# Optimization experiments

Hardware: AMD Instinct MI355X
Metric: run time of the kernel (lower is better)

## Reference

```python
import jax, jax.numpy as jnp
import numpy as np

N = 50000      # nodes
E = 1_600_000  # edges
IN, H, H2, OUT = 256, 128, 64, 2
EPS = 1e-5     # BatchNorm eps


def setup_inputs() -> dict:
    key = jax.random.key(0)
    ks = jax.random.split(key, 18)
    inp = {
        "x": jax.random.normal(ks[0], (N, IN), dtype=jnp.float32),
        "edge_index": jax.random.randint(ks[1], (2, E), 0, N, dtype=jnp.int64),
        # GCNConv 1
        "W1": jax.random.normal(ks[2], (IN, H), dtype=jnp.float32) / np.sqrt(IN),
        "b1": jnp.zeros((H,), dtype=jnp.float32),
        "g1": jnp.ones((H,), dtype=jnp.float32),
        "be1": jnp.zeros((H,), dtype=jnp.float32),
        "m1": jax.random.normal(ks[3], (H,), dtype=jnp.float32) * 0.1,
        "v1": jax.random.uniform(ks[4], (H,), dtype=jnp.float32, minval=0.5, maxval=1.5),
        # GCNConv 2
        "W2": jax.random.normal(ks[5], (H, H2), dtype=jnp.float32) / np.sqrt(H),
        "b2": jnp.zeros((H2,), dtype=jnp.float32),
        "g2": jnp.ones((H2,), dtype=jnp.float32),
        "be2": jnp.zeros((H2,), dtype=jnp.float32),
        "m2": jax.random.normal(ks[6], (H2,), dtype=jnp.float32) * 0.1,
        "v2": jax.random.uniform(ks[7], (H2,), dtype=jnp.float32, minval=0.5, maxval=1.5),
        # final linear
        "Wl": jax.random.normal(ks[8], (H2, OUT), dtype=jnp.float32) / np.sqrt(H2),
        "bl": jnp.zeros((OUT,), dtype=jnp.float32),
    }
    return inp


def _gcn_conv(x, W, b, src, dst, n_nodes):
    # PyG GCNConv: linear transform, then symmetric-normalized aggregation
    # with self-loops (gcn_norm, improved=False, fill_value=1).
    xw = x @ W                                            # [N, H]
    ones = jnp.ones((src.shape[0],), dtype=x.dtype)
    deg = jax.ops.segment_sum(ones, dst, num_segments=n_nodes) + 1.0  # +1 self-loop
    dinv = jax.lax.rsqrt(deg)                             # deg^{-1/2}
    norm = dinv[src] * dinv[dst]                          # [E]
    msgs = xw[src] * norm[:, None]                        # [E, H] gather
    agg = jax.ops.segment_sum(msgs, dst, num_segments=n_nodes)  # scatter-add
    agg = agg + xw * (1.0 / deg)[:, None]                 # self-loop term
    return agg + b


def _bn_relu(x, gamma, beta, mean, var):
    # inference-mode BatchNorm1d + ReLU
    xhat = (x - mean) * jax.lax.rsqrt(var + EPS)
    return jax.nn.relu(xhat * gamma + beta)


def reference(x, edge_index, W1, b1, g1, be1, m1, v1,
              W2, b2, g2, be2, m2, v2, Wl, bl):
    src, dst = edge_index[0], edge_index[1]
    h = _gcn_conv(x, W1, b1, src, dst, N)
    h = _bn_relu(h, g1, be1, m1, v1)
    # dropout is identity in eval mode
    h = _gcn_conv(h, W2, b2, src, dst, N)
    h = _bn_relu(h, g2, be2, m2, v2)
    return h @ Wl + bl
```

## Files before the change

kernel.cpp:

```cpp
#include <hip/hip_runtime.h>

#define N_NODES 50000
#define N_EDGES 1600000
#define IN_F 256
#define H1_F 128
#define H2_F 64
#define OUT_F 2
#define BN_EPS 1e-5f

#define NBUK 782
#define BCAP 3584
#define CHUNK 4096
#define NCHUNK 391
#define NPW 8

typedef __attribute__((ext_vector_type(8))) short bf16x8;
typedef __attribute__((ext_vector_type(4))) float f32x4;
typedef __attribute__((ext_vector_type(4))) int   i32x4;
typedef __attribute__((ext_vector_type(4))) unsigned u32x4;

__device__ __forceinline__ unsigned short f2b(float f) {
    union { float f; unsigned u; } v; v.f = f;
    unsigned r = (v.u + 0x7FFFu + ((v.u >> 16) & 1u)) >> 16;
    return (unsigned short)r;
}
__device__ __forceinline__ float b2f(unsigned short b) {
    union { unsigned u; float f; } v; v.u = ((unsigned)b) << 16;
    return v.f;
}
__device__ __forceinline__ void add2(float& a0, float& a1, unsigned u) {
    union { unsigned u; float f; } lo, hi;
    lo.u = u << 16;
    hi.u = u & 0xFFFF0000u;
    a0 += lo.f; a1 += hi.f;
}

__launch_bounds__(256)
__global__ void chist_kernel(const int* __restrict__ dst, int* __restrict__ h,
                             int* __restrict__ tot) {
    __shared__ int lh[NBUK];
    const int c = blockIdx.x;
    for (int i = threadIdx.x; i < NBUK; i += 256) lh[i] = 0;
    __syncthreads();
    const int e0 = c * CHUNK;
    const int e1 = min(e0 + CHUNK, N_EDGES);
    const i32x4* p = (const i32x4*)(dst + e0);
    const int n4 = (e1 - e0) >> 2;
    for (int i = threadIdx.x; i < n4; i += 256) {
        i32x4 d = __builtin_nontemporal_load(p + i);
        atomicAdd(&lh[d.x >> 6], 1);
        atomicAdd(&lh[d.y >> 6], 1);
        atomicAdd(&lh[d.z >> 6], 1);
        atomicAdd(&lh[d.w >> 6], 1);
    }
    __syncthreads();
    for (int i = threadIdx.x; i < NBUK; i += 256) {
        int v = lh[i];
        h[(size_t)i * NCHUNK + c] = v;
        if (v) atomicAdd(&tot[i], v);
    }
}

__global__ void bscan_kernel(const int* __restrict__ tot, int* __restrict__ boff,
                             int* __restrict__ rowptr) {
    __shared__ int tmp[1024];
    const int t = threadIdx.x;
    int v = (t < NBUK) ? tot[t] : 0;
    tmp[t] = v;
    __syncthreads();
    for (int off = 1; off < 1024; off <<= 1) {
        int a = (t >= off) ? tmp[t - off] : 0;
        __syncthreads();
        tmp[t] += a;
        __syncthreads();
    }
    if (t < NBUK) boff[t] = tmp[t] - v;
    if (t == 0) { boff[NBUK] = N_EDGES; rowptr[N_NODES] = N_EDGES; }
}

__launch_bounds__(256)
__global__ void boffs_kernel(int* __restrict__ h, const int* __restrict__ boff) {
    const int b = (blockIdx.x * blockDim.x + threadIdx.x) >> 6;
    if (b >= NBUK) return;
    const int lane = threadIdx.x & 63;
    int run = boff[b];
    int* row = h + (size_t)b * NCHUNK;
    for (int c0 = 0; c0 < NCHUNK; c0 += 64) {
        int idx = c0 + lane;
        int v = (idx < NCHUNK) ? row[idx] : 0;
        int s = v;
#pragma unroll
        for (int off = 1; off < 64; off <<= 1) {
            int t = __shfl_up(s, off);
            if (lane >= off) s += t;
        }
        if (idx < NCHUNK) row[idx] = run + (s - v);
        run += __shfl(s, 63);
    }
}

__launch_bounds__(256)
__global__ void cscatter_kernel(const int* __restrict__ src, const int* __restrict__ dst,
                                const int* __restrict__ h, unsigned* __restrict__ bedges) {
    __shared__ int cur[NBUK];
    const int c = blockIdx.x;
    for (int i = threadIdx.x; i < NBUK; i += 256) cur[i] = h[(size_t)i * NCHUNK + c];
    __syncthreads();
    const int e0 = c * CHUNK;
    const int e1 = min(e0 + CHUNK, N_EDGES);
    const i32x4* pd = (const i32x4*)(dst + e0);
    const i32x4* ps = (const i32x4*)(src + e0);
    const int n4 = (e1 - e0) >> 2;
    for (int i = threadIdx.x; i < n4; i += 256) {
        i32x4 d = __builtin_nontemporal_load(pd + i);
        i32x4 s = __builtin_nontemporal_load(ps + i);
        int slot;
        slot = atomicAdd(&cur[d.x >> 6], 1); bedges[slot] = (unsigned)s.x | ((unsigned)d.x << 16);
        slot = atomicAdd(&cur[d.y >> 6], 1); bedges[slot] = (unsigned)s.y | ((unsigned)d.y << 16);
        slot = atomicAdd(&cur[d.z >> 6], 1); bedges[slot] = (unsigned)s.z | ((unsigned)d.z << 16);
        slot = atomicAdd(&cur[d.w >> 6], 1); bedges[slot] = (unsigned)s.w | ((unsigned)d.w << 16);
    }
}

__launch_bounds__(256)
__global__ void build_kernel(const unsigned* __restrict__ bedges, const int* __restrict__ boff,
                             unsigned short* __restrict__ perm, int* __restrict__ rowptr,
                             float* __restrict__ dinv) {
    __shared__ unsigned e_lds[BCAP];
    __shared__ unsigned short p_lds[BCAP];
    __shared__ int ncnt[64], ncur[64];

    const int b = blockIdx.x;
    const int t = threadIdx.x;
    const int start = boff[b];
    const int end   = boff[b + 1];
    const int cnt   = end - start;
    const bool fits = (cnt <= BCAP);

    if (t < 64) ncnt[t] = 0;
    __syncthreads();

    for (int i = t; i < cnt; i += 256) {
        unsigned e = bedges[start + i];
        if (fits) e_lds[i] = e;
        atomicAdd(&ncnt[(e >> 16) & 63], 1);
    }
    __syncthreads();

    if (t == 0) {
        int a = 0;
        for (int i = 0; i < 64; ++i) { ncur[i] = a; a += ncnt[i]; }
    }
    __syncthreads();

    if (t < 64) {
        int node = b * 64 + t;
        if (node < N_NODES) {
            rowptr[node] = start + ncur[t];
            dinv[node]   = rsqrtf((float)ncnt[t] + 1.0f);
        }
    }
    __syncthreads();

    for (int i = t; i < cnt; i += 256) {
        unsigned e = fits ? e_lds[i] : bedges[start + i];
        int slot = atomicAdd(&ncur[(e >> 16) & 63], 1);
        unsigned short s = (unsigned short)(e & 0xFFFFu);
        if (fits) p_lds[slot] = s;
        else      perm[start + slot] = s;
    }
    if (fits) {
        __syncthreads();
        for (int i = t; i < cnt; i += 256) perm[start + i] = p_lds[i];
    }
}

__global__ void prep_kernel(const float* __restrict__ W1, const float* __restrict__ W2,
                            unsigned short* __restrict__ w1t, unsigned short* __restrict__ w2t,
                            const float* __restrict__ g1, const float* __restrict__ be1,
                            const float* __restrict__ m1, const float* __restrict__ v1,
                            const float* __restrict__ b1,
                            const float* __restrict__ g2, const float* __restrict__ be2,
                            const float* __restrict__ m2, const float* __restrict__ v2,
                            const float* __restrict__ b2,
                            float* __restrict__ sc1, float* __restrict__ sh1,
                            float* __restrict__ sc2, float* __restrict__ sh2) {
    const int blk = blockIdx.x;
    const int t = threadIdx.x;
    if (blk < 128) {
        int i = blk * 256 + t;
        int n = i / IN_F, k = i % IN_F;
        w1t[i] = f2b(W1[(size_t)k * H1_F + n]);
    } else if (blk < 160) {
        int i = (blk - 128) * 256 + t;
        int n = i / H1_F, k = i % H1_F;
        w2t[i] = f2b(W2[(size_t)k * H2_F + n]);
    } else {
        if (t < H1_F) {
            float s = g1[t] * rsqrtf(v1[t] + BN_EPS);
            sc1[t] = s;
            sh1[t] = (b1[t] - m1[t]) * s + be1[t];
        } else if (t < H1_F + H2_F) {
            int f = t - H1_F;
            float s = g2[f] * rsqrtf(v2[f] + BN_EPS);
            sc2[f] = s;
            sh2[f] = (b2[f] - m2[f]) * s + be2[f];
        }
    }
}

template <int KSTEPS, int NTILES, bool A_BF16>
__launch_bounds__(256)
__global__ void mfma_gemm_kernel(const void* __restrict__ Ap, const unsigned short* __restrict__ BT,
                                 const float* __restrict__ dscale, unsigned short* __restrict__ C,
                                 int M) {
    constexpr int K  = KSTEPS * 32;
    constexpr int NF = NTILES * 16;
    const int wave = threadIdx.x >> 6;
    const int lane = threadIdx.x & 63;
    const int r0   = (blockIdx.x * 4 + wave) * 16;
    const int m    = lane & 15;
    const int kb   = lane >> 4;

    int arow = r0 + m;
    if (arow >= M) arow = M - 1;

    f32x4 acc[NTILES];
#pragma unroll
    for (int nt = 0; nt < NTILES; ++nt) acc[nt] = (f32x4)(0.f);

#pragma unroll
    for (int ks = 0; ks < KSTEPS; ++ks) {
        const int k0 = ks * 32 + kb * 8;
        bf16x8 a;
        if constexpr (A_BF16) {
            a = *(const bf16x8*)((const unsigned short*)Ap + (size_t)arow * K + k0);
        } else {
            const float* af = (const float*)Ap + (size_t)arow * K + k0;
            f32x4 lo = __builtin_nontemporal_load((const f32x4*)af);
            f32x4 hi = __builtin_nontemporal_load((const f32x4*)(af + 4));
            union { bf16x8 v; unsigned short u[8]; } pk;
            pk.u[0] = f2b(lo.x); pk.u[1] = f2b(lo.y); pk.u[2] = f2b(lo.z); pk.u[3] = f2b(lo.w);
            pk.u[4] = f2b(hi.x); pk.u[5] = f2b(hi.y); pk.u[6] = f2b(hi.z); pk.u[7] = f2b(hi.w);
            a = pk.v;
        }
#pragma unroll
        for (int nt = 0; nt < NTILES; ++nt) {
            bf16x8 b = *(const bf16x8*)(BT + (size_t)(nt * 16 + m) * K + k0);
            acc[nt] = __builtin_amdgcn_mfma_f32_16x16x32_bf16(a, b, acc[nt], 0, 0, 0);
        }
    }

#pragma unroll
    for (int reg = 0; reg < 4; ++reg) {
        const int r = r0 + kb * 4 + reg;
        if (r < M) {
            const float ds = dscale[r];
#pragma unroll
            for (int nt = 0; nt < NTILES; ++nt)
                C[(size_t)r * NF + nt * 16 + m] = f2b(acc[nt][reg] * ds);
        }
    }
}

template <int HF, bool FINAL>
__launch_bounds__(256)
__global__ void agg_kernel(const int* __restrict__ rowptr, const unsigned short* __restrict__ perm,
                           const unsigned short* __restrict__ xw, const float* __restrict__ dinv,
                           const float* __restrict__ sc, const float* __restrict__ sh,
                           const float* __restrict__ Wl, const float* __restrict__ bl,
                           void* __restrict__ outp) {
    constexpr int LPE = HF / 8;
    constexpr int G   = 64 / LPE;
    const int wid  = (blockIdx.x * blockDim.x + threadIdx.x) >> 6;
    const int n0   = wid * NPW;
    if (n0 >= N_NODES) return;
    const int lane = threadIdx.x & 63;
    const int grp  = lane / LPE;
    const int fl   = (lane % LPE) * 8;

    f32x4 scl = *(const f32x4*)(sc + fl);
    f32x4 sch = *(const f32x4*)(sc + fl + 4);
    f32x4 shl = *(const f32x4*)(sh + fl);
    f32x4 shh = *(const f32x4*)(sh + fl + 4);
    float wl0[8], wl1[8];
    if constexpr (FINAL) {
#pragma unroll
        for (int i = 0; i < 8; ++i) {
            wl0[i] = Wl[(fl + i) * 2 + 0];
            wl1[i] = Wl[(fl + i) * 2 + 1];
        }
    }

    int rp = 0;
    if (lane <= NPW) rp = rowptr[n0 + lane];
    float dvl = (lane < NPW) ? dinv[n0 + lane] : 0.f;

    for (int k = 0; k < NPW; ++k) {
        const int node  = n0 + k;
        const int start = __shfl(rp, k);
        const int end   = __shfl(rp, k + 1);

        float aA[8];
#pragma unroll
        for (int i = 0; i < 8; ++i) aA[i] = 0.f;

        if (grp == 0) {
            u32x4 u = *(const u32x4*)(xw + (size_t)node * HF + fl);
#pragma unroll
            for (int i = 0; i < 4; ++i) add2(aA[2 * i], aA[2 * i + 1], u[i]);
        }

        for (int base = start; base < end; base += 64) {
            int pidx = base + lane;
            int pv = (int)__builtin_nontemporal_load(perm + (pidx < end ? pidx : end - 1));
            int ne = end - base;
            if (ne > 64) ne = 64;
            if (ne == 64) {
#pragma unroll
                for (int j = 0; j < 64; j += G) {
                    int s = __shfl(pv, j + grp);
                    u32x4 u = *(const u32x4*)(xw + (size_t)s * HF + fl);
#pragma unroll
                    for (int i = 0; i < 4; ++i) add2(aA[2 * i], aA[2 * i + 1], u[i]);
                }
            } else {
                for (int j = 0; j < ne; j += G) {
                    int s = __shfl(pv, j + grp);
                    if (j + grp < ne) {
                        u32x4 u = *(const u32x4*)(xw + (size_t)s * HF + fl);
#pragma unroll
                        for (int i = 0; i < 4; ++i) add2(aA[2 * i], aA[2 * i + 1], u[i]);
                    }
                }
            }
        }

#pragma unroll
        for (int off = LPE; off < 64; off <<= 1)
#pragma unroll
            for (int i = 0; i < 8; ++i) aA[i] += __shfl_xor(aA[i], off);

        const float dv = __shfl(dvl, k);
        float y[8];
#pragma unroll
        for (int i = 0; i < 4; ++i) {
            y[i]     = fmaxf(aA[i] * (dv * scl[i]) + shl[i], 0.f);
            y[i + 4] = fmaxf(aA[i + 4] * (dv * sch[i]) + shh[i], 0.f);
        }

        if constexpr (!FINAL) {
            if (lane < LPE) {
                u32x4 o;
#pragma unroll
                for (int i = 0; i < 4; ++i)
                    o[i] = (unsigned)f2b(y[2 * i]) | ((unsigned)f2b(y[2 * i + 1]) << 16);
                __builtin_nontemporal_store(o, (u32x4*)((unsigned short*)outp + (size_t)node * HF + fl));
            }
        } else {
            float p0 = 0.f, p1 = 0.f;
#pragma unroll
            for (int i = 0; i < 8; ++i) {
                p0 += y[i] * wl0[i];
                p1 += y[i] * wl1[i];
            }
#pragma unroll
            for (int off = 1; off < LPE; off <<= 1) {
                p0 += __shfl_xor(p0, off);
                p1 += __shfl_xor(p1, off);
            }
            if (lane == 0) {
                float* o = (float*)outp;
                o[(size_t)node * 2 + 0] = p0 + bl[0];
                o[(size_t)node * 2 + 1] = p1 + bl[1];
            }
        }
    }
}

extern "C" void kernel_launch(void* const* d_in, const int* in_sizes, int n_in,
                              void* d_out, int out_size, void* d_ws, size_t ws_size,
                              hipStream_t stream) {
    const float* x   = (const float*)d_in[0];
    const int*   ei  = (const int*)d_in[1];
    const float* W1  = (const float*)d_in[2];
    const float* b1  = (const float*)d_in[3];
    const float* g1  = (const float*)d_in[4];
    const float* be1 = (const float*)d_in[5];
    const float* m1  = (const float*)d_in[6];
    const float* v1  = (const float*)d_in[7];
    const float* W2  = (const float*)d_in[8];
    const float* b2  = (const float*)d_in[9];
    const float* g2  = (const float*)d_in[10];
    const float* be2 = (const float*)d_in[11];
    const float* m2  = (const float*)d_in[12];
    const float* v2  = (const float*)d_in[13];
    const float* Wl  = (const float*)d_in[14];
    const float* bl  = (const float*)d_in[15];

    const int* src = ei;
    const int* dst = ei + N_EDGES;

    int*            h      = (int*)d_ws;
    int*            tot    = h + (size_t)NBUK * NCHUNK;
    int*            boff   = tot + 1024;
    int*            rowptr = boff + 1024;
    float*          dinv   = (float*)(rowptr + 50016);
    float*          sc1    = dinv + 50016;
    float*          sh1    = sc1 + 128;
    float*          sc2    = sh1 + 128;
    float*          sh2    = sc2 + 64;
    unsigned*       bedges = (unsigned*)(sh2 + 64);
    unsigned short* perm   = (unsigned short*)(bedges + N_EDGES);
    unsigned short* xwb    = perm + N_EDGES;
    unsigned short* h1b    = xwb + (size_t)N_NODES * H1_F;
    unsigned short* w1t    = h1b + (size_t)N_NODES * H1_F;
    unsigned short* w2t    = w1t + H1_F * IN_F;

    hipMemsetAsync(tot, 0, 1024 * sizeof(int), stream);

    chist_kernel<<<NCHUNK, 256, 0, stream>>>(dst, h, tot);
    bscan_kernel<<<1, 1024, 0, stream>>>(tot, boff, rowptr);
    boffs_kernel<<<(NBUK * 64 + 255) / 256, 256, 0, stream>>>(h, boff);
    cscatter_kernel<<<NCHUNK, 256, 0, stream>>>(src, dst, h, bedges);
    build_kernel<<<NBUK, 256, 0, stream>>>(bedges, boff, perm, rowptr, dinv);

    prep_kernel<<<161, 256, 0, stream>>>(W1, W2, w1t, w2t,
                                         g1, be1, m1, v1, b1,
                                         g2, be2, m2, v2, b2,
                                         sc1, sh1, sc2, sh2);

    mfma_gemm_kernel<IN_F / 32, H1_F / 16, false><<<(N_NODES + 63) / 64, 256, 0, stream>>>(
        x, w1t, dinv, xwb, N_NODES);
    agg_kernel<H1_F, false><<<(N_NODES / NPW + 3) / 4, 256, 0, stream>>>(
        rowptr, perm, xwb, dinv, sc1, sh1, nullptr, nullptr, h1b);

    mfma_gemm_kernel<H1_F / 32, H2_F / 16, true><<<(N_NODES + 63) / 64, 256, 0, stream>>>(
        h1b, w2t, dinv, xwb, N_NODES);
    agg_kernel<H2_F, true><<<(N_NODES / NPW + 3) / 4, 256, 0, stream>>>(
        rowptr, perm, xwb, dinv, sc2, sh2, Wl, bl, (float*)d_out);
}
```

Before: 299.7 us.

## Split layer-1 features into 32-wide chunks for cache-resident gather aggregation

The first GEMM now writes its output in a feature-chunked layout (four 32-feature planes of N×32 bf16), and the layer-1 aggregation runs one grid slice per chunk, so each pass gathers from a ~3.2MB table that fits in cache better. The second GEMM reads this chunked layout directly. Both aggregation kernels switch from 8 nodes per wave to one node per wave. The cost is that edge indices (perm/rowptr) are read four times for layer 1, and with only ~32 edges per node many lanes sit idle per wave.

```diff
diff --git a/kernel.cpp b/kernel.cpp
--- a/kernel.cpp
+++ b/kernel.cpp
@@ -12,7 +12,7 @@
 #define BCAP 3584
 #define CHUNK 4096
 #define NCHUNK 391
-#define NPW 8
+#define FC 32
 
 typedef __attribute__((ext_vector_type(8))) short bf16x8;
 typedef __attribute__((ext_vector_type(4))) float f32x4;
@@ -209,7 +209,7 @@
     }
 }
 
-template <int KSTEPS, int NTILES, bool A_BF16>
+template <int KSTEPS, int NTILES, bool A_CHUNKED, bool CHUNK_OUT>
 __launch_bounds__(256)
 __global__ void mfma_gemm_kernel(const void* __restrict__ Ap, const unsigned short* __restrict__ BT,
                                  const float* __restrict__ dscale, unsigned short* __restrict__ C,
@@ -233,8 +233,9 @@
     for (int ks = 0; ks < KSTEPS; ++ks) {
         const int k0 = ks * 32 + kb * 8;
         bf16x8 a;
-        if constexpr (A_BF16) {
-            a = *(const bf16x8*)((const unsigned short*)Ap + (size_t)arow * K + k0);
+        if constexpr (A_CHUNKED) {
+            a = *(const bf16x8*)((const unsigned short*)Ap +
+                                 (size_t)ks * N_NODES * FC + (size_t)arow * FC + kb * 8);
         } else {
             const float* af = (const float*)Ap + (size_t)arow * K + k0;
             f32x4 lo = __builtin_nontemporal_load((const f32x4*)af);
@@ -257,124 +258,180 @@
         if (r < M) {
             const float ds = dscale[r];
 #pragma unroll
-            for (int nt = 0; nt < NTILES; ++nt)
-                C[(size_t)r * NF + nt * 16 + m] = f2b(acc[nt][reg] * ds);
-        }
-    }
-}
-
-template <int HF, bool FINAL>
-__launch_bounds__(256)
-__global__ void agg_kernel(const int* __restrict__ rowptr, const unsigned short* __restrict__ perm,
-                           const unsigned short* __restrict__ xw, const float* __restrict__ dinv,
-                           const float* __restrict__ sc, const float* __restrict__ sh,
-                           const float* __restrict__ Wl, const float* __restrict__ bl,
-                           void* __restrict__ outp) {
-    constexpr int LPE = HF / 8;
-    constexpr int G   = 64 / LPE;
-    const int wid  = (blockIdx.x * blockDim.x + threadIdx.x) >> 6;
-    const int n0   = wid * NPW;
-    if (n0 >= N_NODES) return;
+            for (int nt = 0; nt < NTILES; ++nt) {
+                if constexpr (CHUNK_OUT) {
+                    C[(size_t)(nt >> 1) * N_NODES * FC + (size_t)r * FC + ((nt & 1) << 4) + m] =
+                        f2b(acc[nt][reg] * ds);
+                } else {
+                    C[(size_t)r * NF + nt * 16 + m] = f2b(acc[nt][reg] * ds);
+                }
+            }
+        }
+    }
+}
+
+__launch_bounds__(256)
+__global__ void agg_chunk_kernel(const int* __restrict__ rowptr, const unsigned short* __restrict__ perm,
+                                 const unsigned short* __restrict__ xw,
+                                 const float* __restrict__ dinv,
+                                 const float* __restrict__ sc, const float* __restrict__ sh,
+                                 unsigned short* __restrict__ out) {
+    const int c = blockIdx.y;
+    const unsigned short* xc = xw + (size_t)c * N_NODES * FC;
+    const int wave = threadIdx.x >> 6;
+    const int node = blockIdx.x * 4 + wave;
+    if (node >= N_NODES) return;
+    const int lane = threadIdx.x & 63;
+    const int grp  = lane >> 2;
+    const int fl   = (lane & 3) << 3;
+
+    float aA[8];
+#pragma unroll
+    for (int i = 0; i < 8; ++i) aA[i] = 0.f;
+
+    if (grp == 0) {
+        u32x4 u = *(const u32x4*)(xc + (size_t)node * FC + fl);
+#pragma unroll
+        for (int i = 0; i < 4; ++i) add2(aA[2 * i], aA[2 * i + 1], u[i]);
+    }
+
+    const int start = rowptr[node];
+    const int end   = rowptr[node + 1];
+    for (int base = start; base < end; base += 64) {
+        int pidx = base + lane;
+        int pv = (int)__builtin_nontemporal_load(perm + (pidx < end ? pidx : end - 1));
+        int ne = end - base;
+        if (ne > 64) ne = 64;
+        if (ne == 64) {
+#pragma unroll
+            for (int j = 0; j < 64; j += 16) {
+                int s = __shfl(pv, j + grp);
+                u32x4 u = *(const u32x4*)(xc + (size_t)s * FC + fl);
+#pragma unroll
+                for (int i = 0; i < 4; ++i) add2(aA[2 * i], aA[2 * i + 1], u[i]);
+            }
+        } else {
+            for (int j = 0; j < ne; j += 16) {
+                int s = __shfl(pv, j + grp);
+                if (j + grp < ne) {
+                    u32x4 u = *(const u32x4*)(xc + (size_t)s * FC + fl);
+#pragma unroll
+                    for (int i = 0; i < 4; ++i) add2(aA[2 * i], aA[2 * i + 1], u[i]);
+                }
+            }
+        }
+    }
+
+#pragma unroll
+    for (int off = 4; off < 64; off <<= 1)
+#pragma unroll
+        for (int i = 0; i < 8; ++i) aA[i] += __shfl_xor(aA[i], off);
+
+    if (lane < 4) {
+        const float dv = dinv[node];
+        const int f = c * FC + fl;
+        f32x4 scl = *(const f32x4*)(sc + f);
+        f32x4 sch = *(const f32x4*)(sc + f + 4);
+        f32x4 shl = *(const f32x4*)(sh + f);
+        f32x4 shh = *(const f32x4*)(sh + f + 4);
+        float y[8];
+#pragma unroll
+        for (int i = 0; i < 4; ++i) {
+            y[i]     = fmaxf(aA[i] * (dv * scl[i]) + shl[i], 0.f);
+            y[i + 4] = fmaxf(aA[i + 4] * (dv * sch[i]) + shh[i], 0.f);
+        }
+        u32x4 o;
+#pragma unroll
+        for (int i = 0; i < 4; ++i)
+            o[i] = (unsigned)f2b(y[2 * i]) | ((unsigned)f2b(y[2 * i + 1]) << 16);
+        __builtin_nontemporal_store(o, (u32x4*)(out + (size_t)c * N_NODES * FC + (size_t)node * FC + fl));
+    }
+}
+
+__launch_bounds__(256)
+__global__ void agg_final_kernel(const int* __restrict__ rowptr, const unsigned short* __restrict__ perm,
+                                 const unsigned short* __restrict__ xw, const float* __restrict__ dinv,
+                                 const float* __restrict__ sc, const float* __restrict__ sh,
+                                 const float* __restrict__ Wl, const float* __restrict__ bl,
+                                 float* __restrict__ outp) {
+    constexpr int HF  = 64;
+    constexpr int LPE = 8;
+    constexpr int G   = 8;
+    const int wave = threadIdx.x >> 6;
+    const int node = blockIdx.x * 4 + wave;
+    if (node >= N_NODES) return;
     const int lane = threadIdx.x & 63;
     const int grp  = lane / LPE;
     const int fl   = (lane % LPE) * 8;
 
+    float aA[8];
+#pragma unroll
+    for (int i = 0; i < 8; ++i) aA[i] = 0.f;
+
+    if (grp == 0) {
+        u32x4 u = *(const u32x4*)(xw + (size_t)node * HF + fl);
+#pragma unroll
+        for (int i = 0; i < 4; ++i) add2(aA[2 * i], aA[2 * i + 1], u[i]);
+    }
+
+    const int start = rowptr[node];
+    const int end   = rowptr[node + 1];
+    for (int base = start; base < end; base += 64) {
+        int pidx = base + lane;
+        int pv = (int)__builtin_nontemporal_load(perm + (pidx < end ? pidx : end - 1));
+        int ne = end - base;
+        if (ne > 64) ne = 64;
+        if (ne == 64) {
+#pragma unroll
+            for (int j = 0; j < 64; j += G) {
+                int s = __shfl(pv, j + grp);
+                u32x4 u = *(const u32x4*)(xw + (size_t)s * HF + fl);
+#pragma unroll
+                for (int i = 0; i < 4; ++i) add2(aA[2 * i], aA[2 * i + 1], u[i]);
+            }
+        } else {
+            for (int j = 0; j < ne; j += G) {
+                int s = __shfl(pv, j + grp);
+                if (j + grp < ne) {
+                    u32x4 u = *(const u32x4*)(xw + (size_t)s * HF + fl);
+#pragma unroll
+                    for (int i = 0; i < 4; ++i) add2(aA[2 * i], aA[2 * i + 1], u[i]);
+                }
+            }
+        }
+    }
+
+#pragma unroll
+    for (int off = LPE; off < 64; off <<= 1)
+#pragma unroll
+        for (int i = 0; i < 8; ++i) aA[i] += __shfl_xor(aA[i], off);
+
+    const float dv = dinv[node];
     f32x4 scl = *(const f32x4*)(sc + fl);
     f32x4 sch = *(const f32x4*)(sc + fl + 4);
     f32x4 shl = *(const f32x4*)(sh + fl);
     f32x4 shh = *(const f32x4*)(sh + fl + 4);
-    float wl0[8], wl1[8];
-    if constexpr (FINAL) {
-#pragma unroll
-        for (int i = 0; i < 8; ++i) {
-            wl0[i] = Wl[(fl + i) * 2 + 0];
-            wl1[i] = Wl[(fl + i) * 2 + 1];
-        }
-    }
-
-    int rp = 0;
-    if (lane <= NPW) rp = rowptr[n0 + lane];
-    float dvl = (lane < NPW) ? dinv[n0 + lane] : 0.f;
-
-    for (int k = 0; k < NPW; ++k) {
-        const int node  = n0 + k;
-        const int start = __shfl(rp, k);
-        const int end   = __shfl(rp, k + 1);
-
-        float aA[8];
-#pragma unroll
-        for (int i = 0; i < 8; ++i) aA[i] = 0.f;
-
-        if (grp == 0) {
-            u32x4 u = *(const u32x4*)(xw + (size_t)node * HF + fl);
-#pragma unroll
-            for (int i = 0; i < 4; ++i) add2(aA[2 * i], aA[2 * i + 1], u[i]);
-        }
-
-        for (int base = start; base < end; base += 64) {
-            int pidx = base + lane;
-            int pv = (int)__builtin_nontemporal_load(perm + (pidx < end ? pidx : end - 1));
-            int ne = end - base;
-            if (ne > 64) ne = 64;
-            if (ne == 64) {
-#pragma unroll
-                for (int j = 0; j < 64; j += G) {
-                    int s = __shfl(pv, j + grp);
-                    u32x4 u = *(const u32x4*)(xw + (size_t)s * HF + fl);
-#pragma unroll
-                    for (int i = 0; i < 4; ++i) add2(aA[2 * i], aA[2 * i + 1], u[i]);
-                }
-            } else {
-                for (int j = 0; j < ne; j += G) {
-                    int s = __shfl(pv, j + grp);
-                    if (j + grp < ne) {
-                        u32x4 u = *(const u32x4*)(xw + (size_t)s * HF + fl);
-#pragma unroll
-                        for (int i = 0; i < 4; ++i) add2(aA[2 * i], aA[2 * i + 1], u[i]);
-                    }
-                }
-            }
-        }
-
-#pragma unroll
-        for (int off = LPE; off < 64; off <<= 1)
-#pragma unroll
-            for (int i = 0; i < 8; ++i) aA[i] += __shfl_xor(aA[i], off);
-
-        const float dv = __shfl(dvl, k);
-        float y[8];
-#pragma unroll
-        for (int i = 0; i < 4; ++i) {
-            y[i]     = fmaxf(aA[i] * (dv * scl[i]) + shl[i], 0.f);
-            y[i + 4] = fmaxf(aA[i + 4] * (dv * sch[i]) + shh[i], 0.f);
-        }
-
-        if constexpr (!FINAL) {
-            if (lane < LPE) {
-                u32x4 o;
-#pragma unroll
-                for (int i = 0; i < 4; ++i)
-                    o[i] = (unsigned)f2b(y[2 * i]) | ((unsigned)f2b(y[2 * i + 1]) << 16);
-                __builtin_nontemporal_store(o, (u32x4*)((unsigned short*)outp + (size_t)node * HF + fl));
-            }
-        } else {
-            float p0 = 0.f, p1 = 0.f;
-#pragma unroll
-            for (int i = 0; i < 8; ++i) {
-                p0 += y[i] * wl0[i];
-                p1 += y[i] * wl1[i];
-            }
-#pragma unroll
-            for (int off = 1; off < LPE; off <<= 1) {
-                p0 += __shfl_xor(p0, off);
-                p1 += __shfl_xor(p1, off);
-            }
-            if (lane == 0) {
-                float* o = (float*)outp;
-                o[(size_t)node * 2 + 0] = p0 + bl[0];
-                o[(size_t)node * 2 + 1] = p1 + bl[1];
-            }
-        }
+    float y[8];
+#pragma unroll
+    for (int i = 0; i < 4; ++i) {
+        y[i]     = fmaxf(aA[i] * (dv * scl[i]) + shl[i], 0.f);
+        y[i + 4] = fmaxf(aA[i + 4] * (dv * sch[i]) + shh[i], 0.f);
+    }
+
+    float p0 = 0.f, p1 = 0.f;
+#pragma unroll
+    for (int i = 0; i < 8; ++i) {
+        p0 += y[i] * Wl[(fl + i) * 2 + 0];
+        p1 += y[i] * Wl[(fl + i) * 2 + 1];
+    }
+#pragma unroll
+    for (int off = 1; off < LPE; off <<= 1) {
+        p0 += __shfl_xor(p0, off);
+        p1 += __shfl_xor(p1, off);
+    }
+    if (lane == 0) {
+        outp[(size_t)node * 2 + 0] = p0 + bl[0];
+        outp[(size_t)node * 2 + 1] = p1 + bl[1];
     }
 }
 
@@ -430,13 +487,13 @@
                                          g2, be2, m2, v2, b2,
                                          sc1, sh1, sc2, sh2);
 
-    mfma_gemm_kernel<IN_F / 32, H1_F / 16, false><<<(N_NODES + 63) / 64, 256, 0, stream>>>(
+    mfma_gemm_kernel<IN_F / 32, H1_F / 16, false, true><<<(N_NODES + 63) / 64, 256, 0, stream>>>(
         x, w1t, dinv, xwb, N_NODES);
-    agg_kernel<H1_F, false><<<(N_NODES / NPW + 3) / 4, 256, 0, stream>>>(
-        rowptr, perm, xwb, dinv, sc1, sh1, nullptr, nullptr, h1b);
-
-    mfma_gemm_kernel<H1_F / 32, H2_F / 16, true><<<(N_NODES + 63) / 64, 256, 0, stream>>>(
+    agg_chunk_kernel<<<dim3((N_NODES + 3) / 4, H1_F / FC), 256, 0, stream>>>(
+        rowptr, perm, xwb, dinv, sc1, sh1, h1b);
+
+    mfma_gemm_kernel<H1_F / 32, H2_F / 16, true, false><<<(N_NODES + 63) / 64, 256, 0, stream>>>(
         h1b, w2t, dinv, xwb, N_NODES);
-    agg_kernel<H2_F, true><<<(N_NODES / NPW + 3) / 4, 256, 0, stream>>>(
+    agg_final_kernel<<<(N_NODES + 3) / 4, 256, 0, stream>>>(
         rowptr, perm, xwb, dinv, sc2, sh2, Wl, bl, (float*)d_out);
 }
```

Measured after the change: 287.2 us. -4.2%, faster.

## Fuse histogram with weight prep, merge bucket scan, one node per wave in aggregation

Applied to the files above, without the earlier changes.

The weight transpose/BN-constant prep blocks are merged into the histogram launch, and the single-block bucket scan is folded into the per-bucket offset kernel, where each wave recomputes its own exclusive prefix from the totals. The aggregation kernels now assign one node per wave instead of eight nodes per wave, giving more waves and better latency hiding for the irregular gathers. This removes two launches and a serial scan stage. In exchange it adds redundant prefix reads in each wave and per-wave overhead for rowptr, dinv and scale loads.

```diff
diff --git a/kernel.cpp b/kernel.cpp
--- a/kernel.cpp
+++ b/kernel.cpp
@@ -12,7 +12,6 @@
 #define BCAP 3584
 #define CHUNK 4096
 #define NCHUNK 391
-#define NPW 8
 
 typedef __attribute__((ext_vector_type(8))) short bf16x8;
 typedef __attribute__((ext_vector_type(4))) float f32x4;
@@ -36,54 +35,83 @@
 }
 
 __launch_bounds__(256)
-__global__ void chist_kernel(const int* __restrict__ dst, int* __restrict__ h,
-                             int* __restrict__ tot) {
-    __shared__ int lh[NBUK];
-    const int c = blockIdx.x;
-    for (int i = threadIdx.x; i < NBUK; i += 256) lh[i] = 0;
-    __syncthreads();
-    const int e0 = c * CHUNK;
-    const int e1 = min(e0 + CHUNK, N_EDGES);
-    const i32x4* p = (const i32x4*)(dst + e0);
-    const int n4 = (e1 - e0) >> 2;
-    for (int i = threadIdx.x; i < n4; i += 256) {
-        i32x4 d = __builtin_nontemporal_load(p + i);
-        atomicAdd(&lh[d.x >> 6], 1);
-        atomicAdd(&lh[d.y >> 6], 1);
-        atomicAdd(&lh[d.z >> 6], 1);
-        atomicAdd(&lh[d.w >> 6], 1);
-    }
-    __syncthreads();
-    for (int i = threadIdx.x; i < NBUK; i += 256) {
-        int v = lh[i];
-        h[(size_t)i * NCHUNK + c] = v;
-        if (v) atomicAdd(&tot[i], v);
-    }
-}
-
-__global__ void bscan_kernel(const int* __restrict__ tot, int* __restrict__ boff,
-                             int* __restrict__ rowptr) {
-    __shared__ int tmp[1024];
-    const int t = threadIdx.x;
-    int v = (t < NBUK) ? tot[t] : 0;
-    tmp[t] = v;
-    __syncthreads();
-    for (int off = 1; off < 1024; off <<= 1) {
-        int a = (t >= off) ? tmp[t - off] : 0;
+__global__ void chist_prep_kernel(const int* __restrict__ dst, int* __restrict__ h,
+                                  int* __restrict__ tot,
+                                  const float* __restrict__ W1, const float* __restrict__ W2,
+                                  unsigned short* __restrict__ w1t, unsigned short* __restrict__ w2t,
+                                  const float* __restrict__ g1, const float* __restrict__ be1,
+                                  const float* __restrict__ m1, const float* __restrict__ v1,
+                                  const float* __restrict__ b1,
+                                  const float* __restrict__ g2, const float* __restrict__ be2,
+                                  const float* __restrict__ m2, const float* __restrict__ v2,
+                                  const float* __restrict__ b2,
+                                  float* __restrict__ sc1, float* __restrict__ sh1,
+                                  float* __restrict__ sc2, float* __restrict__ sh2) {
+    const int blk = blockIdx.x;
+    const int t   = threadIdx.x;
+    if (blk < NCHUNK) {
+        __shared__ int lh[NBUK];
+        const int c = blk;
+        for (int i = t; i < NBUK; i += 256) lh[i] = 0;
         __syncthreads();
-        tmp[t] += a;
+        const int e0 = c * CHUNK;
+        const int e1 = min(e0 + CHUNK, N_EDGES);
+        const i32x4* p = (const i32x4*)(dst + e0);
+        const int n4 = (e1 - e0) >> 2;
+        for (int i = t; i < n4; i += 256) {
+            i32x4 d = __builtin_nontemporal_load(p + i);
+            atomicAdd(&lh[d.x >> 6], 1);
+            atomicAdd(&lh[d.y >> 6], 1);
+            atomicAdd(&lh[d.z >> 6], 1);
+            atomicAdd(&lh[d.w >> 6], 1);
+        }
         __syncthreads();
-    }
-    if (t < NBUK) boff[t] = tmp[t] - v;
-    if (t == 0) { boff[NBUK] = N_EDGES; rowptr[N_NODES] = N_EDGES; }
-}
-
-__launch_bounds__(256)
-__global__ void boffs_kernel(int* __restrict__ h, const int* __restrict__ boff) {
+        for (int i = t; i < NBUK; i += 256) {
+            int v = lh[i];
+            h[(size_t)i * NCHUNK + c] = v;
+            if (v) atomicAdd(&tot[i], v);
+        }
+    } else {
+        const int blk2 = blk - NCHUNK;
+        if (blk2 < 128) {
+            int i = blk2 * 256 + t;
+            int n = i / IN_F, k = i % IN_F;
+            w1t[i] = f2b(W1[(size_t)k * H1_F + n]);
+        } else if (blk2 < 160) {
+            int i = (blk2 - 128) * 256 + t;
+            int n = i / H1_F, k = i % H1_F;
+            w2t[i] = f2b(W2[(size_t)k * H2_F + n]);
+        } else {
+            if (t < H1_F) {
+                float s = g1[t] * rsqrtf(v1[t] + BN_EPS);
+                sc1[t] = s;
+                sh1[t] = (b1[t] - m1[t]) * s + be1[t];
+            } else if (t < H1_F + H2_F) {
+                int f = t - H1_F;
+                float s = g2[f] * rsqrtf(v2[f] + BN_EPS);
+                sc2[f] = s;
+                sh2[f] = (b2[f] - m2[f]) * s + be2[f];
+            }
+        }
+    }
+}
+
+__launch_bounds__(256)
+__global__ void scanoffs_kernel(const int* __restrict__ tot, int* __restrict__ boff,
+                                int* __restrict__ h, int* __restrict__ rowptr) {
     const int b = (blockIdx.x * blockDim.x + threadIdx.x) >> 6;
     if (b >= NBUK) return;
     const int lane = threadIdx.x & 63;
-    int run = boff[b];
+
+    int acc = 0;
+    for (int i = lane; i < NBUK; i += 64)
+        if (i < b) acc += tot[i];
+#pragma unroll
+    for (int off = 1; off < 64; off <<= 1) acc += __shfl_xor(acc, off);
+    if (lane == 0) boff[b] = acc;
+    if (b == 0 && lane == 0) { boff[NBUK] = N_EDGES; rowptr[N_NODES] = N_EDGES; }
+
+    int run = acc;
     int* row = h + (size_t)b * NCHUNK;
     for (int c0 = 0; c0 < NCHUNK; c0 += 64) {
         int idx = c0 + lane;
@@ -91,8 +119,8 @@
         int s = v;
 #pragma unroll
         for (int off = 1; off < 64; off <<= 1) {
-            int t = __shfl_up(s, off);
-            if (lane >= off) s += t;
+            int t2 = __shfl_up(s, off);
+            if (lane >= off) s += t2;
         }
         if (idx < NCHUNK) row[idx] = run + (s - v);
         run += __shfl(s, 63);
@@ -175,40 +203,6 @@
     }
 }
 
-__global__ void prep_kernel(const float* __restrict__ W1, const float* __restrict__ W2,
-                            unsigned short* __restrict__ w1t, unsigned short* __restrict__ w2t,
-                            const float* __restrict__ g1, const float* __restrict__ be1,
-                            const float* __restrict__ m1, const float* __restrict__ v1,
-                            const float* __restrict__ b1,
-                            const float* __restrict__ g2, const float* __restrict__ be2,
-                            const float* __restrict__ m2, const float* __restrict__ v2,
-                            const float* __restrict__ b2,
-                            float* __restrict__ sc1, float* __restrict__ sh1,
-                            float* __restrict__ sc2, float* __restrict__ sh2) {
-    const int blk = blockIdx.x;
-    const int t = threadIdx.x;
-    if (blk < 128) {
-        int i = blk * 256 + t;
-        int n = i / IN_F, k = i % IN_F;
-        w1t[i] = f2b(W1[(size_t)k * H1_F + n]);
-    } else if (blk < 160) {
-        int i = (blk - 128) * 256 + t;
-        int n = i / H1_F, k = i % H1_F;
-        w2t[i] = f2b(W2[(size_t)k * H2_F + n]);
-    } else {
-        if (t < H1_F) {
-            float s = g1[t] * rsqrtf(v1[t] + BN_EPS);
-            sc1[t] = s;
-            sh1[t] = (b1[t] - m1[t]) * s + be1[t];
-        } else if (t < H1_F + H2_F) {
-            int f = t - H1_F;
-            float s = g2[f] * rsqrtf(v2[f] + BN_EPS);
-            sc2[f] = s;
-            sh2[f] = (b2[f] - m2[f]) * s + be2[f];
-        }
-    }
-}
-
 template <int KSTEPS, int NTILES, bool A_BF16>
 __launch_bounds__(256)
 __global__ void mfma_gemm_kernel(const void* __restrict__ Ap, const unsigned short* __restrict__ BT,
@@ -272,108 +266,91 @@
                            void* __restrict__ outp) {
     constexpr int LPE = HF / 8;
     constexpr int G   = 64 / LPE;
-    const int wid  = (blockIdx.x * blockDim.x + threadIdx.x) >> 6;
-    const int n0   = wid * NPW;
-    if (n0 >= N_NODES) return;
+    const int wave = threadIdx.x >> 6;
+    const int node = blockIdx.x * 4 + wave;
+    if (node >= N_NODES) return;
     const int lane = threadIdx.x & 63;
     const int grp  = lane / LPE;
     const int fl   = (lane % LPE) * 8;
 
+    float aA[8];
+#pragma unroll
+    for (int i = 0; i < 8; ++i) aA[i] = 0.f;
+
+    if (grp == 0) {
+        u32x4 u = *(const u32x4*)(xw + (size_t)node * HF + fl);
+#pragma unroll
+        for (int i = 0; i < 4; ++i) add2(aA[2 * i], aA[2 * i + 1], u[i]);
+    }
+
+    const int start = rowptr[node];
+    const int end   = rowptr[node + 1];
+    for (int base = start; base < end; base += 64) {
+        int pidx = base + lane;
+        int pv = (int)__builtin_nontemporal_load(perm + (pidx < end ? pidx : end - 1));
+        int ne = end - base;
+        if (ne > 64) ne = 64;
+        if (ne == 64) {
+#pragma unroll
+            for (int j = 0; j < 64; j += G) {
+                int s = __shfl(pv, j + grp);
+                u32x4 u = *(const u32x4*)(xw + (size_t)s * HF + fl);
+#pragma unroll
+                for (int i = 0; i < 4; ++i) add2(aA[2 * i], aA[2 * i + 1], u[i]);
+            }
+        } else {
+            for (int j = 0; j < ne; j += G) {
+                int s = __shfl(pv, j + grp);
+                if (j + grp < ne) {
+                    u32x4 u = *(const u32x4*)(xw + (size_t)s * HF + fl);
+#pragma unroll
+                    for (int i = 0; i < 4; ++i) add2(aA[2 * i], aA[2 * i + 1], u[i]);
+                }
+            }
+        }
+    }
+
+#pragma unroll
+    for (int off = LPE; off < 64; off <<= 1)
+#pragma unroll
+        for (int i = 0; i < 8; ++i) aA[i] += __shfl_xor(aA[i], off);
+
+    const float dv = dinv[node];
     f32x4 scl = *(const f32x4*)(sc + fl);
     f32x4 sch = *(const f32x4*)(sc + fl + 4);
     f32x4 shl = *(const f32x4*)(sh + fl);
     f32x4 shh = *(const f32x4*)(sh + fl + 4);
-    float wl0[8], wl1[8];
-    if constexpr (FINAL) {
+    float y[8];
+#pragma unroll
+    for (int i = 0; i < 4; ++i) {
+        y[i]     = fmaxf(aA[i] * (dv * scl[i]) + shl[i], 0.f);
+        y[i + 4] = fmaxf(aA[i + 4] * (dv * sch[i]) + shh[i], 0.f);
+    }
+
+    if constexpr (!FINAL) {
+        if (lane < LPE) {
+            u32x4 o;
+#pragma unroll
+            for (int i = 0; i < 4; ++i)
+                o[i] = (unsigned)f2b(y[2 * i]) | ((unsigned)f2b(y[2 * i + 1]) << 16);
+            __builtin_nontemporal_store(o, (u32x4*)((unsigned short*)outp + (size_t)node * HF + fl));
+        }
+    } else {
+        float p0 = 0.f, p1 = 0.f;
 #pragma unroll
         for (int i = 0; i < 8; ++i) {
-            wl0[i] = Wl[(fl + i) * 2 + 0];
-            wl1[i] = Wl[(fl + i) * 2 + 1];
-        }
-    }
-
-    int rp = 0;
-    if (lane <= NPW) rp = rowptr[n0 + lane];
-    float dvl = (lane < NPW) ? dinv[n0 + lane] : 0.f;
-
-    for (int k = 0; k < NPW; ++k) {
-        const int node  = n0 + k;
-        const int start = __shfl(rp, k);
-        const int end   = __shfl(rp, k + 1);
-
-        float aA[8];
-#pragma unroll
-        for (int i = 0; i < 8; ++i) aA[i] = 0.f;
-
-        if (grp == 0) {
-            u32x4 u = *(const u32x4*)(xw + (size_t)node * HF + fl);
-#pragma unroll
-            for (int i = 0; i < 4; ++i) add2(aA[2 * i], aA[2 * i + 1], u[i]);
-        }
-
-        for (int base = start; base < end; base += 64) {
-            int pidx = base + lane;
-            int pv = (int)__builtin_nontemporal_load(perm + (pidx < end ? pidx : end - 1));
-            int ne = end - base;
-            if (ne > 64) ne = 64;
-            if (ne == 64) {
-#pragma unroll
-                for (int j = 0; j < 64; j += G) {
-                    int s = __shfl(pv, j + grp);
-                    u32x4 u = *(const u32x4*)(xw + (size_t)s * HF + fl);
-#pragma unroll
-                    for (int i = 0; i < 4; ++i) add2(aA[2 * i], aA[2 * i + 1], u[i]);
-                }
-            } else {
-                for (int j = 0; j < ne; j += G) {
-                    int s = __shfl(pv, j + grp);
-                    if (j + grp < ne) {
-                        u32x4 u = *(const u32x4*)(xw + (size_t)s * HF + fl);
-#pragma unroll
-                        for (int i = 0; i < 4; ++i) add2(aA[2 * i], aA[2 * i + 1], u[i]);
-                    }
-                }
-            }
-        }
-
-#pragma unroll
-        for (int off = LPE; off < 64; off <<= 1)
-#pragma unroll
-            for (int i = 0; i < 8; ++i) aA[i] += __shfl_xor(aA[i], off);
-
-        const float dv = __shfl(dvl, k);
-        float y[8];
-#pragma unroll
-        for (int i = 0; i < 4; ++i) {
-            y[i]     = fmaxf(aA[i] * (dv * scl[i]) + shl[i], 0.f);
-            y[i + 4] = fmaxf(aA[i + 4] * (dv * sch[i]) + shh[i], 0.f);
-        }
-
-        if constexpr (!FINAL) {
-            if (lane < LPE) {
-                u32x4 o;
-#pragma unroll
-                for (int i = 0; i < 4; ++i)
-                    o[i] = (unsigned)f2b(y[2 * i]) | ((unsigned)f2b(y[2 * i + 1]) << 16);
-                __builtin_nontemporal_store(o, (u32x4*)((unsigned short*)outp + (size_t)node * HF + fl));
-            }
-        } else {
-            float p0 = 0.f, p1 = 0.f;
-#pragma unroll
-            for (int i = 0; i < 8; ++i) {
-                p0 += y[i] * wl0[i];
-                p1 += y[i] * wl1[i];
-            }
-#pragma unroll
-            for (int off = 1; off < LPE; off <<= 1) {
-                p0 += __shfl_xor(p0, off);
-                p1 += __shfl_xor(p1, off);
-            }
-            if (lane == 0) {
-                float* o = (float*)outp;
-                o[(size_t)node * 2 + 0] = p0 + bl[0];
-                o[(size_t)node * 2 + 1] = p1 + bl[1];
-            }
+            p0 += y[i] * Wl[(fl + i) * 2 + 0];
+            p1 += y[i] * Wl[(fl + i) * 2 + 1];
+        }
+#pragma unroll
+        for (int off = 1; off < LPE; off <<= 1) {
+            p0 += __shfl_xor(p0, off);
+            p1 += __shfl_xor(p1, off);
+        }
+        if (lane == 0) {
+            float* o = (float*)outp;
+            o[(size_t)node * 2 + 0] = p0 + bl[0];
+            o[(size_t)node * 2 + 1] = p1 + bl[1];
         }
     }
 }
@@ -419,24 +396,22 @@
 
     hipMemsetAsync(tot, 0, 1024 * sizeof(int), stream);
 
-    chist_kernel<<<NCHUNK, 256, 0, stream>>>(dst, h, tot);
-    bscan_kernel<<<1, 1024, 0, stream>>>(tot, boff, rowptr);
-    boffs_kernel<<<(NBUK * 64 + 255) / 256, 256, 0, stream>>>(h, boff);
+    chist_prep_kernel<<<NCHUNK + 161, 256, 0, stream>>>(dst, h, tot,
+                                                        W1, W2, w1t, w2t,
+                                                        g1, be1, m1, v1, b1,
+                                                        g2, be2, m2, v2, b2,
+                                                        sc1, sh1, sc2, sh2);
+    scanoffs_kernel<<<(NBUK * 64 + 255) / 256, 256, 0, stream>>>(tot, boff, h, rowptr);
     cscatter_kernel<<<NCHUNK, 256, 0, stream>>>(src, dst, h, bedges);
     build_kernel<<<NBUK, 256, 0, stream>>>(bedges, boff, perm, rowptr, dinv);
 
-    prep_kernel<<<161, 256, 0, stream>>>(W1, W2, w1t, w2t,
-                                         g1, be1, m1, v1, b1,
-                                         g2, be2, m2, v2, b2,
-                                         sc1, sh1, sc2, sh2);
-
     mfma_gemm_kernel<IN_F / 32, H1_F / 16, false><<<(N_NODES + 63) / 64, 256, 0, stream>>>(
         x, w1t, dinv, xwb, N_NODES);
-    agg_kernel<H1_F, false><<<(N_NODES / NPW + 3) / 4, 256, 0, stream>>>(
+    agg_kernel<H1_F, false><<<(N_NODES + 3) / 4, 256, 0, stream>>>(
         rowptr, perm, xwb, dinv, sc1, sh1, nullptr, nullptr, h1b);
 
     mfma_gemm_kernel<H1_F / 32, H2_F / 16, true><<<(N_NODES + 63) / 64, 256, 0, stream>>>(
         h1b, w2t, dinv, xwb, N_NODES);
-    agg_kernel<H2_F, true><<<(N_NODES / NPW + 3) / 4, 256, 0, stream>>>(
+    agg_kernel<H2_F, true><<<(N_NODES + 3) / 4, 256, 0, stream>>>(
         rowptr, perm, xwb, dinv, sc2, sh2, Wl, bl, (float*)d_out);
 }
```

Result: faster. 254.0 us (median of 2 runs) (-15.2%).
